# Kernel tuning notes

Hardware: AMD Instinct MI355X
Metric: run time of the kernel (lower is better)

Reference implementation:

```python
import jax, jax.numpy as jnp
import numpy as np

N_NODES = 50000
N_EDGES = 800000
N_GRAPHS = 512
IN_CH, H, OUT = 58, 64, 128
HEADS1 = 4
NEG_SLOPE = 0.2
BN_EPS = 1e-5


def setup_inputs() -> dict:
    key = jax.random.key(0)
    ks = jax.random.split(key, 16)
    x = jax.random.normal(ks[0], (N_NODES, IN_CH), dtype=jnp.float32)
    edge_index = jax.random.randint(ks[1], (2, N_EDGES), 0, N_NODES, dtype=jnp.int64)
    batch = jnp.sort(jax.random.randint(ks[2], (N_NODES,), 0, N_GRAPHS, dtype=jnp.int64))
    s = 0.1
    return {
        "x": x,
        "edge_index": edge_index,
        "batch": batch,
        "W1": jax.random.normal(ks[3], (IN_CH, HEADS1 * H), dtype=jnp.float32) * s,
        "att_src1": jax.random.normal(ks[4], (HEADS1, H), dtype=jnp.float32) * s,
        "att_dst1": jax.random.normal(ks[5], (HEADS1, H), dtype=jnp.float32) * s,
        "b1": jnp.zeros((HEADS1 * H,), dtype=jnp.float32),
        "W2": jax.random.normal(ks[6], (HEADS1 * H, OUT), dtype=jnp.float32) * s,
        "att_src2": jax.random.normal(ks[7], (1, OUT), dtype=jnp.float32) * s,
        "att_dst2": jax.random.normal(ks[8], (1, OUT), dtype=jnp.float32) * s,
        "b2": jnp.zeros((OUT,), dtype=jnp.float32),
        "gamma": jax.random.normal(ks[9], (OUT,), dtype=jnp.float32) * 0.1 + 1.0,
        "beta": jax.random.normal(ks[10], (OUT,), dtype=jnp.float32) * 0.1,
    }


def gat_conv(x, src, dst, W, att_src, att_dst, b, heads, d_out):
    """PyG GATConv (concat=True, dropout off), self-loops already in src/dst."""
    n = x.shape[0]
    h = (x @ W).reshape(n, heads, d_out)                 # [N,H,D]
    a_s = jnp.einsum("nhd,hd->nh", h, att_src)            # [N,H]
    a_d = jnp.einsum("nhd,hd->nh", h, att_dst)            # [N,H]
    e = jax.nn.leaky_relu(a_s[src] + a_d[dst], NEG_SLOPE)  # [E,H]
    # softmax over edges grouped by destination node
    m = jax.ops.segment_max(e, dst, num_segments=n)
    ex = jnp.exp(e - m[dst])
    z = jax.ops.segment_sum(ex, dst, num_segments=n)
    alpha = ex / (z[dst] + 1e-16)
    msg = h[src] * alpha[:, :, None]                      # [E,H,D]
    out = jax.ops.segment_sum(msg, dst, num_segments=n)   # [N,H,D]
    return out.reshape(n, heads * d_out) + b


def reference(x, edge_index, batch, W1, att_src1, att_dst1, b1,
              W2, att_src2, att_dst2, b2, gamma, beta):
    n = x.shape[0]
    loops = jnp.arange(n, dtype=edge_index.dtype)
    src = jnp.concatenate([edge_index[0], loops])
    dst = jnp.concatenate([edge_index[1], loops])

    h1 = jax.nn.relu(gat_conv(x, src, dst, W1, att_src1, att_dst1, b1, HEADS1, H))
    h2 = jax.nn.relu(gat_conv(h1, src, dst, W2, att_src2, att_dst2, b2, 1, OUT))

    # global mean pool over graphs
    sums = jax.ops.segment_sum(h2, batch, num_segments=N_GRAPHS)      # [G,OUT]
    cnt = jax.ops.segment_sum(jnp.ones((n,), h2.dtype), batch, num_segments=N_GRAPHS)
    pooled = sums / jnp.maximum(cnt, 1.0)[:, None]

    # BatchNorm1d, training mode (batch statistics, biased variance)
    mu = pooled.mean(axis=0)
    var = pooled.var(axis=0)
    return (pooled - mu) / jnp.sqrt(var + BN_EPS) * gamma + beta
```

## Files before the change

### kernel.cpp

```cpp
#include <hip/hip_runtime.h>
#include <hip/hip_bf16.h>
#include <math.h>

#define N_NODES  50000
#define N_EDGES  800000
#define E_TOT    850000
#define N_GRAPHS 512
#define IN_CH    58
#define K1P      64
#define C1       256
#define H1       4
#define C2       128
#define NEG_SLOPE 0.2f
#define SLOT_CAP 64
#define NBUILD   208
#define NATT     3125

typedef __attribute__((ext_vector_type(8))) short short8;
typedef __attribute__((ext_vector_type(4))) float f32x4;

__device__ __forceinline__ float lo16(unsigned u) { return __uint_as_float(u << 16); }
__device__ __forceinline__ float hi16(unsigned u) { return __uint_as_float(u & 0xffff0000u); }
__device__ __forceinline__ float leaky(float e) { return e > 0.f ? e : NEG_SLOPE * e; }
__device__ __forceinline__ unsigned short f2bfu(float v) {
    __hip_bfloat16 b = __float2bfloat16(v);
    return *(unsigned short*)&b;
}
__device__ __forceinline__ unsigned pack2(float lo, float hi) {
    return (unsigned)f2bfu(lo) | ((unsigned)f2bfu(hi) << 16);
}

__global__ __launch_bounds__(256) void k_frontA(const float* __restrict__ W1,
                                                const float* __restrict__ W2,
                                                const float* __restrict__ atts1,
                                                const float* __restrict__ attd1,
                                                unsigned short* __restrict__ w1p,
                                                unsigned short* __restrict__ w2p,
                                                float* __restrict__ wproj) {
    int b = blockIdx.x;
    int t = threadIdx.x;
    if (b < 256) {
        if (t < K1P) {
            float v = (t < IN_CH) ? W1[t * C1 + b] : 0.f;
            int h = b >> 6, jj = (b >> 4) & 3, l15 = b & 15;
            int kk = t >> 5, quad = (t >> 3) & 3, e = t & 7;
            int f = (h * 4 + jj) * 2 + kk;
            w1p[(f * 64 + l15 * 4 + quad) * 8 + e] = f2bfu(v);
        }
    } else if (b < 384) {
        int n = b - 256;
        int j = n >> 4, l15 = n & 15;
        int k0 = t >> 5, quad = (t >> 3) & 3, e = t & 7;
        int f = j * 8 + k0;
        w2p[(f * 64 + l15 * 4 + quad) * 8 + e] = f2bfu(W2[t * C2 + n]);
    } else {
        int k = t >> 2, h = t & 3;
        float s = 0.f, dd = 0.f;
        if (k < IN_CH) {
            for (int j = 0; j < 64; ++j) {
                float wv = W1[k * C1 + h * 64 + j];
                s  += wv * atts1[h * 64 + j];
                dd += wv * attd1[h * 64 + j];
            }
        }
        wproj[t] = s;
        wproj[256 + t] = dd;
    }
}

__global__ __launch_bounds__(256) void k_mid(const int* __restrict__ src,
                                             const int* __restrict__ dst,
                                             int* __restrict__ deg,
                                             int* __restrict__ slots,
                                             const float* __restrict__ x,
                                             const float* __restrict__ wproj,
                                             unsigned short* __restrict__ xbf,
                                             float* __restrict__ a_s,
                                             float* __restrict__ a_d) {
    int b = blockIdx.x;
    int t = threadIdx.x;
    if (b < NBUILD) {
        int j0 = (b * 256 + t) * 16;
        int s[16], d[16], pos[16];
        bool v[16];
#pragma unroll
        for (int k = 0; k < 16; ++k) {
            int j = j0 + k;
            v[k] = j < E_TOT;
            if (v[k]) {
                if (j < N_EDGES) { s[k] = src[j]; d[k] = dst[j]; }
                else             { s[k] = d[k] = j - N_EDGES; }
            }
        }
#pragma unroll
        for (int k = 0; k < 16; ++k)
            if (v[k]) pos[k] = atomicAdd(&deg[d[k]], 1);
#pragma unroll
        for (int k = 0; k < 16; ++k)
            if (v[k]) slots[(d[k] << 6) + pos[k]] = s[k];
    } else {
        int wave = t >> 6, lane = t & 63;
        int q = lane >> 4, hl = lane & 15;
        int n = (b - NBUILD) * 16 + wave * 4 + q;
        float xa[4] = {0.f, 0.f, 0.f, 0.f};
        const float* xr = x + (size_t)n * IN_CH + hl * 4;
        if (hl < 14) {
            float4 xv = *(const float4*)xr;
            xa[0] = xv.x; xa[1] = xv.y; xa[2] = xv.z; xa[3] = xv.w;
        } else if (hl == 14) {
            xa[0] = xr[0]; xa[1] = xr[1];
        }
        ((uint2*)xbf)[n * 16 + hl] = make_uint2(pack2(xa[0], xa[1]), pack2(xa[2], xa[3]));
        float ps[4] = {0.f, 0.f, 0.f, 0.f}, pd[4] = {0.f, 0.f, 0.f, 0.f};
#pragma unroll
        for (int cc = 0; cc < 4; ++cc) {
            int c = hl * 4 + cc;
            float4 wsv = *(const float4*)(wproj + c * 4);
            float4 wdv = *(const float4*)(wproj + 256 + c * 4);
            ps[0] += xa[cc] * wsv.x; ps[1] += xa[cc] * wsv.y;
            ps[2] += xa[cc] * wsv.z; ps[3] += xa[cc] * wsv.w;
            pd[0] += xa[cc] * wdv.x; pd[1] += xa[cc] * wdv.y;
            pd[2] += xa[cc] * wdv.z; pd[3] += xa[cc] * wdv.w;
        }
#pragma unroll
        for (int o = 8; o > 0; o >>= 1) {
#pragma unroll
            for (int r = 0; r < 4; ++r) {
                ps[r] += __shfl_down(ps[r], o, 16);
                pd[r] += __shfl_down(pd[r], o, 16);
            }
        }
        if (hl == 0) {
            *(float4*)(a_s + n * 4) = make_float4(ps[0], ps[1], ps[2], ps[3]);
            *(float4*)(a_d + n * 4) = make_float4(pd[0], pd[1], pd[2], pd[3]);
        }
    }
}

__global__ __launch_bounds__(256) void k_l1_agg(const int* __restrict__ degv,
                                                const int* __restrict__ slots,
                                                const float* __restrict__ a_s,
                                                const float* __restrict__ a_d,
                                                const uint2* __restrict__ xbf,
                                                unsigned short* __restrict__ xagg) {
    int t = threadIdx.x;
    int wave = t >> 6, lane = t & 63;
    int q = lane >> 4, hl = lane & 15;
    int d = blockIdx.x * 16 + wave * 4 + q;
    int beg = d << 6;
    int deg = degv[d];
    float4 ad = *(const float4*)(a_d + d * 4);
    float z0 = 0.f, z1 = 0.f, z2 = 0.f, z3 = 0.f;
    float a0[4] = {0.f, 0.f, 0.f, 0.f};
    float a1[4] = {0.f, 0.f, 0.f, 0.f};
    float a2[4] = {0.f, 0.f, 0.f, 0.f};
    float a3[4] = {0.f, 0.f, 0.f, 0.f};
    int i = 0;
    for (; i + 8 <= deg; i += 8) {
        int e0 = beg + i;
        int s[8]; uint2 u[8]; float4 as[8];
#pragma unroll
        for (int k = 0; k < 8; ++k) s[k] = slots[e0 + k];
#pragma unroll
        for (int k = 0; k < 8; ++k) u[k] = xbf[s[k] * 16 + hl];
#pragma unroll
        for (int k = 0; k < 8; ++k) as[k] = *(const float4*)(a_s + s[k] * 4);
#pragma unroll
        for (int k = 0; k < 8; ++k) {
            float e0h = __expf(leaky(as[k].x + ad.x));
            float e1h = __expf(leaky(as[k].y + ad.y));
            float e2h = __expf(leaky(as[k].z + ad.z));
            float e3h = __expf(leaky(as[k].w + ad.w));
            z0 += e0h; z1 += e1h; z2 += e2h; z3 += e3h;
            float c0 = lo16(u[k].x), c1 = hi16(u[k].x);
            float c2 = lo16(u[k].y), c3 = hi16(u[k].y);
            a0[0] += e0h * c0; a0[1] += e0h * c1; a0[2] += e0h * c2; a0[3] += e0h * c3;
            a1[0] += e1h * c0; a1[1] += e1h * c1; a1[2] += e1h * c2; a1[3] += e1h * c3;
            a2[0] += e2h * c0; a2[1] += e2h * c1; a2[2] += e2h * c2; a2[3] += e2h * c3;
            a3[0] += e3h * c0; a3[1] += e3h * c1; a3[2] += e3h * c2; a3[3] += e3h * c3;
        }
    }
    for (; i < deg; ++i) {
        int s = slots[beg + i];
        uint2 u = xbf[s * 16 + hl];
        float4 as = *(const float4*)(a_s + s * 4);
        float e0h = __expf(leaky(as.x + ad.x));
        float e1h = __expf(leaky(as.y + ad.y));
        float e2h = __expf(leaky(as.z + ad.z));
        float e3h = __expf(leaky(as.w + ad.w));
        z0 += e0h; z1 += e1h; z2 += e2h; z3 += e3h;
        float c0 = lo16(u.x), c1 = hi16(u.x);
        float c2 = lo16(u.y), c3 = hi16(u.y);
        a0[0] += e0h * c0; a0[1] += e0h * c1; a0[2] += e0h * c2; a0[3] += e0h * c3;
        a1[0] += e1h * c0; a1[1] += e1h * c1; a1[2] += e1h * c2; a1[3] += e1h * c3;
        a2[0] += e2h * c0; a2[1] += e2h * c1; a2[2] += e2h * c2; a2[3] += e2h * c3;
        a3[0] += e3h * c0; a3[1] += e3h * c1; a3[2] += e3h * c2; a3[3] += e3h * c3;
    }
    float i0 = 1.f / z0, i1 = 1.f / z1, i2 = 1.f / z2, i3 = 1.f / z3;
    int T = d >> 4, r = d & 15;
    int kk = hl >> 3, qd = (hl >> 1) & 3, half = hl & 1;
    uint2* xo = (uint2*)xagg;
    int base = (((T * 8 + kk) * 64) + r * 4 + qd) * 2 + half;
    xo[base +   0] = make_uint2(pack2(a0[0] * i0, a0[1] * i0), pack2(a0[2] * i0, a0[3] * i0));
    xo[base + 256] = make_uint2(pack2(a1[0] * i1, a1[1] * i1), pack2(a1[2] * i1, a1[3] * i1));
    xo[base + 512] = make_uint2(pack2(a2[0] * i2, a2[1] * i2), pack2(a2[2] * i2, a2[3] * i2));
    xo[base + 768] = make_uint2(pack2(a3[0] * i3, a3[1] * i3), pack2(a3[2] * i3, a3[3] * i3));
}

__global__ __launch_bounds__(256) void k_gemm12(const unsigned short* __restrict__ xagg,
                                                const unsigned short* __restrict__ w1p,
                                                const float* __restrict__ b1v,
                                                const unsigned short* __restrict__ w2p,
                                                const float* __restrict__ atts,
                                                const float* __restrict__ attd,
                                                unsigned short* __restrict__ h2bf,
                                                float* __restrict__ a_s,
                                                float* __restrict__ a_d) {
    __shared__ unsigned short hlds[4][16][264];
    int t = threadIdx.x;
    int wave = t >> 6, lane = t & 63;
    int T = blockIdx.x * 4 + wave;
    int m0 = T * 16;
    int l15 = lane & 15, quad = lane >> 4;
    int fl = l15 * 4 + quad;
    bool active = m0 < N_NODES;

    if (active) {
        const short8* xf  = (const short8*)xagg + (size_t)T * 512 + fl;
        const short8* w1f = (const short8*)w1p + fl;
        short8 av[H1][2];
#pragma unroll
        for (int h = 0; h < H1; ++h) {
            av[h][0] = xf[(h * 2 + 0) * 64];
            av[h][1] = xf[(h * 2 + 1) * 64];
        }
#pragma unroll
        for (int h = 0; h < H1; ++h) {
            short8 wb0[4], wb1[4];
#pragma unroll
            for (int jj = 0; jj < 4; ++jj) {
                wb0[jj] = w1f[(((h * 4 + jj) * 2) + 0) * 64];
                wb1[jj] = w1f[(((h * 4 + jj) * 2) + 1) * 64];
            }
            f32x4 acc[4];
#pragma unroll
            for (int jj = 0; jj < 4; ++jj) {
                acc[jj] = (f32x4){0.f, 0.f, 0.f, 0.f};
                acc[jj] = __builtin_amdgcn_mfma_f32_16x16x32_bf16(av[h][0], wb0[jj], acc[jj], 0, 0, 0);
                acc[jj] = __builtin_amdgcn_mfma_f32_16x16x32_bf16(av[h][1], wb1[jj], acc[jj], 0, 0, 0);
            }
#pragma unroll
            for (int jj = 0; jj < 4; ++jj) {
                int c = h * 64 + jj * 16 + l15;
                float bb = b1v[c];
#pragma unroll
                for (int r = 0; r < 4; ++r)
                    hlds[wave][quad * 4 + r][c] = f2bfu(fmaxf(acc[jj][r] + bb, 0.f));
            }
        }
    }
    __syncthreads();
    if (!active) return;

    short8 a2[8];
    const unsigned short* a2row = &hlds[wave][l15][0] + quad * 8;
#pragma unroll
    for (int k0 = 0; k0 < 8; ++k0) a2[k0] = *(const short8*)(a2row + k0 * 32);

    const short8* w2f = (const short8*)w2p + fl;
    unsigned short* scr = &hlds[wave][0][0];
    float ps[4] = {0.f, 0.f, 0.f, 0.f}, pd[4] = {0.f, 0.f, 0.f, 0.f};
#pragma unroll
    for (int j = 0; j < 8; ++j) {
        short8 wb[8];
#pragma unroll
        for (int k0 = 0; k0 < 8; ++k0)
            wb[k0] = w2f[(j * 8 + k0) * 64];
        f32x4 acc = (f32x4){0.f, 0.f, 0.f, 0.f};
#pragma unroll
        for (int k0 = 0; k0 < 8; ++k0)
            acc = __builtin_amdgcn_mfma_f32_16x16x32_bf16(a2[k0], wb[k0], acc, 0, 0, 0);
        float as_ = atts[j * 16 + l15], ad_ = attd[j * 16 + l15];
#pragma unroll
        for (int r = 0; r < 4; ++r) {
            float v = acc[r];
            scr[(quad * 4 + r) * 136 + j * 16 + l15] = f2bfu(v);
            ps[r] += v * as_;
            pd[r] += v * ad_;
        }
    }
#pragma unroll
    for (int r = 0; r < 4; ++r) {
#pragma unroll
        for (int o = 8; o > 0; o >>= 1) {
            ps[r] += __shfl_down(ps[r], o, 16);
            pd[r] += __shfl_down(pd[r], o, 16);
        }
        if (l15 == 0) {
            int n = m0 + quad * 4 + r;
            a_s[n] = ps[r];
            a_d[n] = pd[r];
        }
    }
    int row = lane >> 2, seg = lane & 3;
#pragma unroll
    for (int c = 0; c < 4; ++c) {
        short8 v = *(const short8*)(scr + row * 136 + (c * 4 + seg) * 8);
        *(short8*)(h2bf + (size_t)(m0 + row) * C2 + (c * 4 + seg) * 8) = v;
    }
}

__global__ __launch_bounds__(256) void k_l2_aggpool(const int* __restrict__ degv,
                                                    const int* __restrict__ slots,
                                                    const float* __restrict__ a_s,
                                                    const float* __restrict__ a_d,
                                                    const unsigned short* __restrict__ h2bf,
                                                    const float* __restrict__ b2,
                                                    const int* __restrict__ batch,
                                                    float* __restrict__ pooled) {
    __shared__ float sacc[8][C2];
    __shared__ int sg[8];
    int t = threadIdx.x;
    int wave = t >> 6, lane = t & 63;
    int half = lane >> 5, hl = lane & 31;
    int nodeIdx = wave * 2 + half;
    int d = blockIdx.x * 8 + nodeIdx;
    int beg = d << 6;
    int deg = degv[d];
    float ad = a_d[d];
    const uint2* rows = (const uint2*)h2bf;
    float a0 = 0.f, a1 = 0.f, a2 = 0.f, a3 = 0.f, z = 0.f;
    int i = 0;
    for (; i + 8 <= deg; i += 8) {
        int e0 = beg + i;
        int s[8]; uint2 u[8]; float ex[8];
#pragma unroll
        for (int k = 0; k < 8; ++k) s[k] = slots[e0 + k];
#pragma unroll
        for (int k = 0; k < 8; ++k) u[k] = rows[s[k] * 32 + hl];
#pragma unroll
        for (int k = 0; k < 8; ++k) ex[k] = __expf(leaky(a_s[s[k]] + ad));
#pragma unroll
        for (int k = 0; k < 8; ++k) {
            z  += ex[k];
            a0 += ex[k] * lo16(u[k].x); a1 += ex[k] * hi16(u[k].x);
            a2 += ex[k] * lo16(u[k].y); a3 += ex[k] * hi16(u[k].y);
        }
    }
    for (; i < deg; ++i) {
        int s = slots[beg + i];
        uint2 u = rows[s * 32 + hl];
        float ex = __expf(leaky(a_s[s] + ad));
        z  += ex;
        a0 += ex * lo16(u.x); a1 += ex * hi16(u.x);
        a2 += ex * lo16(u.y); a3 += ex * hi16(u.y);
    }
    float inv = 1.f / z;
    int c = hl * 4;
    float4 bv = *(const float4*)(b2 + c);
    float v0 = fmaxf(a0 * inv + bv.x, 0.f);
    float v1 = fmaxf(a1 * inv + bv.y, 0.f);
    float v2 = fmaxf(a2 * inv + bv.z, 0.f);
    float v3 = fmaxf(a3 * inv + bv.w, 0.f);
    if (hl == 0) sg[nodeIdx] = batch[d];
    *(float4*)&sacc[nodeIdx][c] = make_float4(v0, v1, v2, v3);
    __syncthreads();
    if (t < C2) {
        float run = sacc[0][t];
        int gprev = sg[0];
#pragma unroll
        for (int j = 1; j < 8; ++j) {
            int gj = sg[j];
            float v = sacc[j][t];
            if (gj == gprev) {
                run += v;
            } else {
                atomicAdd(&pooled[gprev * C2 + t], run);
                run = v;
                gprev = gj;
            }
        }
        atomicAdd(&pooled[gprev * C2 + t], run);
    }
}

__global__ __launch_bounds__(512) void k_bn(const float* __restrict__ pooled,
                                            const int* __restrict__ batch,
                                            const float* __restrict__ gamma,
                                            const float* __restrict__ beta,
                                            float* __restrict__ out) {
    int c = blockIdx.x;
    int g = threadIdx.x;
    int lo = 0, hi = N_NODES;
    while (lo < hi) { int m = (lo + hi) >> 1; if (batch[m] < g) lo = m + 1; else hi = m; }
    int lo2 = lo, hi2 = N_NODES;
    while (lo2 < hi2) { int m = (lo2 + hi2) >> 1; if (batch[m] < g + 1) lo2 = m + 1; else hi2 = m; }
    float cntg = (float)(hi2 - lo);

    __shared__ float red[512];
    __shared__ float s_mu, s_var;
    float v = pooled[g * C2 + c] / fmaxf(cntg, 1.0f);
    red[g] = v;
    __syncthreads();
    for (int s = 256; s > 0; s >>= 1) {
        if (g < s) red[g] += red[g + s];
        __syncthreads();
    }
    if (g == 0) s_mu = red[0] * (1.0f / N_GRAPHS);
    __syncthreads();
    float dv = v - s_mu;
    red[g] = dv * dv;
    __syncthreads();
    for (int s = 256; s > 0; s >>= 1) {
        if (g < s) red[g] += red[g + s];
        __syncthreads();
    }
    if (g == 0) s_var = red[0] * (1.0f / N_GRAPHS);
    __syncthreads();
    out[g * C2 + c] = dv * rsqrtf(s_var + 1e-5f) * gamma[c] + beta[c];
}

extern "C" void kernel_launch(void* const* d_in, const int* in_sizes, int n_in,
                              void* d_out, int out_size, void* d_ws, size_t ws_size,
                              hipStream_t stream) {
    const float* x     = (const float*)d_in[0];
    const int*   eidx  = (const int*)d_in[1];
    const int*   batch = (const int*)d_in[2];
    const float* W1    = (const float*)d_in[3];
    const float* atts1 = (const float*)d_in[4];
    const float* attd1 = (const float*)d_in[5];
    const float* b1    = (const float*)d_in[6];
    const float* W2    = (const float*)d_in[7];
    const float* atts2 = (const float*)d_in[8];
    const float* attd2 = (const float*)d_in[9];
    const float* b2    = (const float*)d_in[10];
    const float* gamma = (const float*)d_in[11];
    const float* beta  = (const float*)d_in[12];
    float* out = (float*)d_out;
    float* ws  = (float*)d_ws;

    const int* src = eidx;
    const int* dst = eidx + N_EDGES;

    const size_t o_xbf    = 0;
    const size_t o_xagg   = 1600000;
    const size_t o_h2bf   = 8000000;
    const size_t o_w1p    = 11200000;
    const size_t o_w2p    = 11208192;
    const size_t o_wproj  = 11224576;
    const size_t o_as1    = 11225088;
    const size_t o_ad1    = 11425088;
    const size_t o_as2    = 11625088;
    const size_t o_ad2    = 11675088;
    const size_t o_slots  = 11725088;
    const size_t o_deg    = 14925088;
    const size_t o_pool   = 14975088;
    const size_t total    = 15040624;

    int* p_slots = (int*)(ws + o_slots);
    int* p_deg   = (int*)(ws + o_deg);
    unsigned short* p_xbf  = (unsigned short*)(ws + o_xbf);
    unsigned short* p_xagg = (unsigned short*)(ws + o_xagg);
    unsigned short* p_h2bf = (unsigned short*)(ws + o_h2bf);
    unsigned short* p_w1p  = (unsigned short*)(ws + o_w1p);
    unsigned short* p_w2p  = (unsigned short*)(ws + o_w2p);

    hipMemsetAsync(ws + o_deg, 0, (total - o_deg) * sizeof(float), stream);

    k_frontA<<<385, 256, 0, stream>>>(W1, W2, atts1, attd1,
                                      p_w1p, p_w2p, ws + o_wproj);
    k_mid<<<NBUILD + NATT, 256, 0, stream>>>(src, dst, p_deg, p_slots,
                                             x, ws + o_wproj, p_xbf,
                                             ws + o_as1, ws + o_ad1);

    const int nagg1 = N_NODES / 16;
    const int nagg2 = N_NODES / 8;
    const int nmfma = (N_NODES + 63) / 64;

    k_l1_agg<<<nagg1, 256, 0, stream>>>(p_deg, p_slots, ws + o_as1, ws + o_ad1,
                                        (const uint2*)p_xbf, p_xagg);
    k_gemm12<<<nmfma, 256, 0, stream>>>(p_xagg, p_w1p, b1, p_w2p, atts2, attd2,
                                        p_h2bf, ws + o_as2, ws + o_ad2);

    k_l2_aggpool<<<nagg2, 256, 0, stream>>>(p_deg, p_slots, ws + o_as2, ws + o_ad2,
                                            p_h2bf, b2, batch, ws + o_pool);

    k_bn<<<C2, 512, 0, stream>>>(ws + o_pool, batch, gamma, beta, out);
}
```

Baseline: 260.4 us.

## Build CSR slots via two-pass bucketed scatter with shared-memory atomics

The edge-to-slot build no longer does a global atomicAdd per edge on the degree array. Edges are now binned into 196 destination buckets of 256 nodes each: k_mid uses a shared-memory histogram, reserves space with one global atomic per bucket, and writes (src,dst) pairs into a bucket buffer. A new k_scat kernel then scatters each bucket into the slots using shared-memory atomics and writes the degrees. The goal is to cut global atomic contention and make the slot writes more local. The cost is an extra kernel launch and an extra write and read of the edges through the bucket buffer, which reuses the xagg region.

```diff
diff --git a/kernel.cpp b/kernel.cpp
--- a/kernel.cpp
+++ b/kernel.cpp
@@ -15,6 +15,8 @@
 #define SLOT_CAP 64
 #define NBUILD   208
 #define NATT     3125
+#define NBUCK    196
+#define BCAP     5120
 
 typedef __attribute__((ext_vector_type(8))) short short8;
 typedef __attribute__((ext_vector_type(4))) float f32x4;
@@ -70,18 +72,22 @@
 
 __global__ __launch_bounds__(256) void k_mid(const int* __restrict__ src,
                                              const int* __restrict__ dst,
-                                             int* __restrict__ deg,
-                                             int* __restrict__ slots,
+                                             int* __restrict__ bcnt,
+                                             uint2* __restrict__ ebuf,
                                              const float* __restrict__ x,
                                              const float* __restrict__ wproj,
                                              unsigned short* __restrict__ xbf,
                                              float* __restrict__ a_s,
                                              float* __restrict__ a_d) {
+    __shared__ int lhist[NBUCK];
+    __shared__ int lbase[NBUCK];
     int b = blockIdx.x;
     int t = threadIdx.x;
     if (b < NBUILD) {
+        if (t < NBUCK) lhist[t] = 0;
+        __syncthreads();
         int j0 = (b * 256 + t) * 16;
-        int s[16], d[16], pos[16];
+        int s[16], d[16], bk[16], lp[16];
         bool v[16];
 #pragma unroll
         for (int k = 0; k < 16; ++k) {
@@ -90,14 +96,20 @@
             if (v[k]) {
                 if (j < N_EDGES) { s[k] = src[j]; d[k] = dst[j]; }
                 else             { s[k] = d[k] = j - N_EDGES; }
+                bk[k] = d[k] >> 8;
             }
         }
 #pragma unroll
         for (int k = 0; k < 16; ++k)
-            if (v[k]) pos[k] = atomicAdd(&deg[d[k]], 1);
+            if (v[k]) lp[k] = atomicAdd(&lhist[bk[k]], 1);
+        __syncthreads();
+        if (t < NBUCK) lbase[t] = atomicAdd(&bcnt[t], lhist[t]);
+        __syncthreads();
 #pragma unroll
         for (int k = 0; k < 16; ++k)
-            if (v[k]) slots[(d[k] << 6) + pos[k]] = s[k];
+            if (v[k])
+                ebuf[(size_t)bk[k] * BCAP + lbase[bk[k]] + lp[k]] =
+                    make_uint2((unsigned)s[k], (unsigned)d[k]);
     } else {
         int wave = t >> 6, lane = t & 63;
         int q = lane >> 4, hl = lane & 15;
@@ -135,6 +147,37 @@
             *(float4*)(a_d + n * 4) = make_float4(pd[0], pd[1], pd[2], pd[3]);
         }
     }
+}
+
+__global__ __launch_bounds__(256) void k_scat(const int* __restrict__ bcnt,
+                                              const uint2* __restrict__ ebuf,
+                                              int* __restrict__ deg,
+                                              int* __restrict__ slots) {
+    __shared__ int ldeg[256];
+    int blk = blockIdx.x, t = threadIdx.x;
+    ldeg[t] = 0;
+    __syncthreads();
+    int cnt = bcnt[blk];
+    const uint2* eb = ebuf + (size_t)blk * BCAP;
+    int base = 0;
+    for (; base + 1024 <= cnt; base += 1024) {
+        uint2 e[4];
+#pragma unroll
+        for (int k = 0; k < 4; ++k) e[k] = eb[base + k * 256 + t];
+#pragma unroll
+        for (int k = 0; k < 4; ++k) {
+            int pos = atomicAdd(&ldeg[e[k].y & 255], 1);
+            slots[((int)e[k].y << 6) + pos] = (int)e[k].x;
+        }
+    }
+    for (int i = base + t; i < cnt; i += 256) {
+        uint2 e = eb[i];
+        int pos = atomicAdd(&ldeg[e.y & 255], 1);
+        slots[((int)e.y << 6) + pos] = (int)e.x;
+    }
+    __syncthreads();
+    int g = (blk << 8) + t;
+    if (g < N_NODES) deg[g] = ldeg[t];
 }
 
 __global__ __launch_bounds__(256) void k_l1_agg(const int* __restrict__ degv,
@@ -455,10 +498,13 @@
     const size_t o_slots  = 11725088;
     const size_t o_deg    = 14925088;
     const size_t o_pool   = 14975088;
-    const size_t total    = 15040624;
+    const size_t o_bcnt   = 15040624;
+    const size_t total    = 15040880;
 
     int* p_slots = (int*)(ws + o_slots);
     int* p_deg   = (int*)(ws + o_deg);
+    int* p_bcnt  = (int*)(ws + o_bcnt);
+    uint2* p_ebuf = (uint2*)(ws + o_xagg);
     unsigned short* p_xbf  = (unsigned short*)(ws + o_xbf);
     unsigned short* p_xagg = (unsigned short*)(ws + o_xagg);
     unsigned short* p_h2bf = (unsigned short*)(ws + o_h2bf);
@@ -469,9 +515,10 @@
 
     k_frontA<<<385, 256, 0, stream>>>(W1, W2, atts1, attd1,
                                       p_w1p, p_w2p, ws + o_wproj);
-    k_mid<<<NBUILD + NATT, 256, 0, stream>>>(src, dst, p_deg, p_slots,
+    k_mid<<<NBUILD + NATT, 256, 0, stream>>>(src, dst, p_bcnt, p_ebuf,
                                              x, ws + o_wproj, p_xbf,
                                              ws + o_as1, ws + o_ad1);
+    k_scat<<<NBUCK, 256, 0, stream>>>(p_bcnt, p_ebuf, p_deg, p_slots);
 
     const int nagg1 = N_NODES / 16;
     const int nagg2 = N_NODES / 8;
```

New measurement: 244.5 us. 1.07x faster.
